# Kernel tuning notes

Hardware: AMD Instinct MI355X
Metric: run time of the kernel (lower is better)

## Reference

```python
import jax, jax.numpy as jnp
import numpy as np

B, T, C, H = 4, 2048, 1024, 1024

def setup_inputs() -> dict:
    key = jax.random.key(0)
    ks = jax.random.split(key, 7)
    s = 0.02
    return {
        "x": jax.random.normal(ks[0], (B, T, C), dtype=jnp.float32),
        "k": jax.random.normal(ks[1], (B, T, C), dtype=jnp.float32),
        "q": jax.random.normal(ks[2], (B, T, C), dtype=jnp.float32),
        "v": jax.random.normal(ks[3], (B, T, C), dtype=jnp.float32),
        "Wk": jax.random.normal(ks[4], (C, H), dtype=jnp.float32) * s,
        "Wq": jax.random.normal(ks[5], (C, H), dtype=jnp.float32) * s,
        "Wv": jax.random.normal(ks[6], (C, H), dtype=jnp.float32) * s,
    }

def reference(x, k, q, v, Wk, Wq, Wv):
    Tcur = x.shape[1]
    kp = jnp.einsum('btc,ch->bth', k, Wk)
    qp = jnp.einsum('btc,ch->bth', q, Wq)
    # NOTE: original torch code (faithfully) projects v with the QUERY weights
    vp = jnp.einsum('btc,ch->bth', v, Wq)
    scale = jnp.asarray(H, jnp.float32) ** -0.5
    weights = jnp.einsum('bth,bsh->bts', qp, kp) * scale  # [B,T,T]
    causal = jnp.tril(jnp.ones((Tcur, Tcur), dtype=bool))
    weights = jnp.where(causal, weights, -jnp.inf)
    weights = jax.nn.softmax(weights, axis=-1)
    # dropout p=0.0 -> identity
    out = jnp.einsum('bts,bsh->bth', weights, vp)
    return out
```

## Files before the change

### kernel.cpp

```cpp
#include <hip/hip_runtime.h>
#include <stdint.h>
#include <math.h>

typedef unsigned short u16;
typedef __attribute__((ext_vector_type(8))) short short8;
typedef __attribute__((ext_vector_type(8))) u16 ushort8;
typedef __attribute__((ext_vector_type(4))) u16 u16x4;
typedef __attribute__((ext_vector_type(4))) float floatx4;

__device__ __forceinline__ u16 f2bf(float f) {
  union { float f; unsigned u; } c; c.f = f;
  unsigned u = c.u;
  return (u16)((u + 0x7fffu + ((u >> 16) & 1u)) >> 16);
}
__device__ __forceinline__ float bf2f(u16 h) {
  union { unsigned u; float f; } c; c.u = (unsigned)h << 16;
  return c.f;
}

__device__ __forceinline__ void async16(const u16* g, u16* l) {
  auto* gp = reinterpret_cast<const __attribute__((address_space(1))) uint32_t*>(
      reinterpret_cast<uintptr_t>(g));
  auto* lp = reinterpret_cast<__attribute__((address_space(3))) uint32_t*>(
      reinterpret_cast<uintptr_t>(l));
  __builtin_amdgcn_global_load_lds(gp, lp, 16, 0, 0);
}

#define WAIT_VM4 0xF74
#define WAIT_VM0 0xF70

template <int OUT_BF16>
__global__ __launch_bounds__(256) void gemm_bt(
    const u16* __restrict__ A, const u16* __restrict__ B, void* __restrict__ Cv,
    int K, int lda, int ldb, int ldc,
    long long sA, long long sB, long long sC,
    float scale, int tri_grid, int causal_klimit, int rev_m,
    int vpt, u16* __restrict__ vpC) {
  int bm, bn;
  if (tri_grid) {
    const int bx = blockIdx.x;
    int i = (int)((sqrtf(8.f * bx + 1.f) - 1.f) * 0.5f);
    while ((i + 1) * (i + 2) / 2 <= bx) ++i;
    while (i * (i + 1) / 2 > bx) --i;
    bm = i;
    bn = bx - i * (i + 1) / 2;
  } else {
    bm = rev_m ? ((int)gridDim.x - 1 - (int)blockIdx.x) : (int)blockIdx.x;
    bn = blockIdx.y;
  }
  const int m0 = bm * 128;
  const int n0 = bn * 128;
  A += (size_t)blockIdx.z * sA;
  B += (size_t)blockIdx.z * sB;

  __shared__ u16 As[2][4096];
  __shared__ u16 Bs[2][4096];

  const int tid = threadIdx.x;
  const int lane = tid & 63;
  const int wid = tid >> 6;
  const int wm = (wid & 1) * 64;
  const int wn = (wid >> 1) * 64;
  const int fr = lane & 15;
  const int fq = lane >> 4;

  floatx4 acc[4][4] = {};

  int kt_end = K >> 5;
  if (causal_klimit) {
    int lim = (m0 >> 5) + 4;
    if (lim < kt_end) kt_end = lim;
  }

  const int rowi = tid >> 2;
  const int segi = tid & 3;
  const int sgz = segi ^ ((rowi >> 1) & 3);
  const u16* gA = A + (size_t)(m0 + rowi) * lda + sgz * 8;
  const u16* gB = B + (size_t)(n0 + rowi) * ldb + sgz * 8;

  int offA[4], offB[4];
#pragma unroll
  for (int i = 0; i < 4; ++i) {
    int ra = wm + i * 16 + fr;
    offA[i] = ra * 32 + (fq ^ ((ra >> 1) & 3)) * 8;
    int rb = wn + i * 16 + fr;
    offB[i] = rb * 32 + (fq ^ ((rb >> 1) & 3)) * 8;
  }

  auto issue = [&](int kt) {
    const int k0 = kt << 5;
    const int odd = kt & 1;
    async16(gA + k0, &As[odd][tid * 8]);
    async16(gA + k0 + (size_t)64 * lda, &As[odd][tid * 8 + 2048]);
    async16(gB + k0, &Bs[odd][tid * 8]);
    async16(gB + k0 + (size_t)64 * ldb, &Bs[odd][tid * 8 + 2048]);
  };

  issue(0);
  for (int kt = 0; kt < kt_end; ++kt) {
    if (kt + 1 < kt_end) {
      issue(kt + 1);
      __builtin_amdgcn_s_waitcnt(WAIT_VM4);
    } else {
      __builtin_amdgcn_s_waitcnt(WAIT_VM0);
    }
    asm volatile("s_barrier" ::: "memory");

    const u16* ab = As[kt & 1];
    const u16* bb = Bs[kt & 1];
    short8 av[4], bv[4];
#pragma unroll
    for (int i = 0; i < 4; ++i) av[i] = *(const short8*)(ab + offA[i]);
#pragma unroll
    for (int j = 0; j < 4; ++j) bv[j] = *(const short8*)(bb + offB[j]);

#pragma unroll
    for (int i = 0; i < 4; ++i)
#pragma unroll
      for (int j = 0; j < 4; ++j)
        acc[i][j] = __builtin_amdgcn_mfma_f32_16x16x32_bf16(av[i], bv[j],
                                                            acc[i][j], 0, 0, 0);
    asm volatile("s_barrier" ::: "memory");
  }

  if (vpt && blockIdx.z == 2) {
#pragma unroll
    for (int i = 0; i < 4; ++i) {
      const int m = m0 + wm + i * 16 + fq * 4;
      const int b = m >> 11, t = m & 2047;
#pragma unroll
      for (int j = 0; j < 4; ++j) {
        const int n = n0 + wn + j * 16 + fr;
        u16x4 o;
#pragma unroll
        for (int r = 0; r < 4; ++r) o[r] = f2bf(acc[i][j][r]);
        *(u16x4*)&vpC[(size_t)b * 2097152 + (size_t)n * 2048 + t] = o;
      }
    }
    return;
  }
  if (OUT_BF16) {
    u16* C = (u16*)Cv + (size_t)blockIdx.z * sC;
#pragma unroll
    for (int i = 0; i < 4; ++i) {
      const int m = m0 + wm + i * 16 + fq * 4;
#pragma unroll
      for (int j = 0; j < 4; ++j) {
        const int n = n0 + wn + j * 16 + fr;
#pragma unroll
        for (int r = 0; r < 4; ++r)
          C[(size_t)(m + r) * ldc + n] = f2bf(acc[i][j][r] * scale);
      }
    }
  } else {
    float* C = (float*)Cv + (size_t)blockIdx.z * sC;
#pragma unroll
    for (int i = 0; i < 4; ++i) {
      const int m = m0 + wm + i * 16 + fq * 4;
#pragma unroll
      for (int j = 0; j < 4; ++j) {
        const int n = n0 + wn + j * 16 + fr;
#pragma unroll
        for (int r = 0; r < 4; ++r)
          C[(size_t)(m + r) * ldc + n] = acc[i][j][r] * scale;
      }
    }
  }
}

__global__ __launch_bounds__(512, 2) void gemm_bt_256(
    const u16* __restrict__ A, const u16* __restrict__ B,
    u16* __restrict__ Cb, int K, int lda, int ldb, int ldc,
    long long sA, long long sB, long long sC, u16* __restrict__ vpC) {
  const int m0 = blockIdx.x * 256;
  const int n0 = blockIdx.y * 256;
  A += (size_t)blockIdx.z * sA;
  B += (size_t)blockIdx.z * sB;

  __shared__ u16 lds[2][32768];

  const int tid = threadIdx.x;
  const int lane = tid & 63;
  const int wid = tid >> 6;
  const int wr = wid & 1;
  const int wc = wid >> 1;
  const int fr = lane & 15;
  const int fq = lane >> 4;

  floatx4 acc[8][4] = {};
  const int NT = K >> 6;

  const int srow = tid >> 3;
  const int sseg = (tid & 7) ^ (srow & 7);
  const u16* gA = A + (size_t)(m0 + srow) * lda + sseg * 8;
  const u16* gB = B + (size_t)(n0 + srow) * ldb + sseg * 8;
  const int ldst = tid * 8;

  auto stageA = [&](int h, int t) {
    u16* d = &lds[t & 1][h * 8192 + ldst];
    const u16* s = gA + (size_t)(h * 128) * lda + t * 64;
    async16(s, d);
    async16(s + (size_t)64 * lda, d + 4096);
  };
  auto stageB = [&](int h, int t) {
    u16* d = &lds[t & 1][16384 + h * 8192 + ldst];
    const u16* s = gB + (size_t)(h * 128) * ldb + t * 64;
    async16(s, d);
    async16(s + (size_t)64 * ldb, d + 4096);
  };

  int aoff[2], boff[2];
#pragma unroll
  for (int s = 0; s < 2; ++s) {
    const int seg = ((((s << 2) + fq) ^ (fr & 7))) * 8;
    aoff[s] = wr * 8192 + fr * 64 + seg;
    boff[s] = 16384 + (wc >> 1) * 8192 + (wc & 1) * 4096 + fr * 64 + seg;
  }

  stageA(0, 0); stageA(1, 0); stageB(0, 0); stageB(1, 0);
  stageB(0, 1); stageB(1, 1);
  __builtin_amdgcn_s_waitcnt(WAIT_VM4);
  asm volatile("s_barrier" ::: "memory");

  short8 a[4][2], b0[2][2], b1[2][2];
  for (int t = 0; t < NT; ++t) {
    const u16* L = lds[t & 1];

#pragma unroll
    for (int i = 0; i < 4; ++i)
#pragma unroll
      for (int s = 0; s < 2; ++s)
        a[i][s] = *(const short8*)(L + aoff[s] + i * 1024);
#pragma unroll
    for (int j = 0; j < 2; ++j)
#pragma unroll
      for (int s = 0; s < 2; ++s)
        b0[j][s] = *(const short8*)(L + boff[s] + j * 1024);
    if (t + 1 < NT) stageA(0, t + 1);
    asm volatile("s_barrier" ::: "memory");
    __builtin_amdgcn_s_setprio(1);
#pragma unroll
    for (int i = 0; i < 4; ++i)
#pragma unroll
      for (int j = 0; j < 2; ++j) {
        acc[i][j] = __builtin_amdgcn_mfma_f32_16x16x32_bf16(
            a[i][0], b0[j][0], acc[i][j], 0, 0, 0);
        acc[i][j] = __builtin_amdgcn_mfma_f32_16x16x32_bf16(
            a[i][1], b0[j][1], acc[i][j], 0, 0, 0);
      }
    __builtin_amdgcn_s_setprio(0);
    asm volatile("s_barrier" ::: "memory");

#pragma unroll
    for (int j = 0; j < 2; ++j)
#pragma unroll
      for (int s = 0; s < 2; ++s)
        b1[j][s] = *(const short8*)(L + boff[s] + (2 + j) * 1024);
    if (t + 1 < NT) stageA(1, t + 1);
    asm volatile("s_barrier" ::: "memory");
    __builtin_amdgcn_s_setprio(1);
#pragma unroll
    for (int i = 0; i < 4; ++i)
#pragma unroll
      for (int j = 0; j < 2; ++j) {
        acc[i][2 + j] = __builtin_amdgcn_mfma_f32_16x16x32_bf16(
            a[i][0], b1[j][0], acc[i][2 + j], 0, 0, 0);
        acc[i][2 + j] = __builtin_amdgcn_mfma_f32_16x16x32_bf16(
            a[i][1], b1[j][1], acc[i][2 + j], 0, 0, 0);
      }
    __builtin_amdgcn_s_setprio(0);
    asm volatile("s_barrier" ::: "memory");

#pragma unroll
    for (int i = 0; i < 4; ++i)
#pragma unroll
      for (int s = 0; s < 2; ++s)
        a[i][s] = *(const short8*)(L + aoff[s] + (4 + i) * 1024);
    if (t + 2 < NT) stageB(0, t + 2);
    asm volatile("s_barrier" ::: "memory");
    __builtin_amdgcn_s_setprio(1);
#pragma unroll
    for (int i = 0; i < 4; ++i)
#pragma unroll
      for (int j = 0; j < 2; ++j) {
        acc[4 + i][j] = __builtin_amdgcn_mfma_f32_16x16x32_bf16(
            a[i][0], b0[j][0], acc[4 + i][j], 0, 0, 0);
        acc[4 + i][j] = __builtin_amdgcn_mfma_f32_16x16x32_bf16(
            a[i][1], b0[j][1], acc[4 + i][j], 0, 0, 0);
      }
    __builtin_amdgcn_s_setprio(0);
    asm volatile("s_barrier" ::: "memory");

    if (t + 2 < NT) {
      stageB(1, t + 2);
      __builtin_amdgcn_s_waitcnt(WAIT_VM4);
    } else {
      __builtin_amdgcn_s_waitcnt(WAIT_VM0);
    }
    asm volatile("s_barrier" ::: "memory");
    __builtin_amdgcn_s_setprio(1);
#pragma unroll
    for (int i = 0; i < 4; ++i)
#pragma unroll
      for (int j = 0; j < 2; ++j) {
        acc[4 + i][2 + j] = __builtin_amdgcn_mfma_f32_16x16x32_bf16(
            a[i][0], b1[j][0], acc[4 + i][2 + j], 0, 0, 0);
        acc[4 + i][2 + j] = __builtin_amdgcn_mfma_f32_16x16x32_bf16(
            a[i][1], b1[j][1], acc[4 + i][2 + j], 0, 0, 0);
      }
    __builtin_amdgcn_s_setprio(0);
    asm volatile("s_barrier" ::: "memory");
  }

  const int mBase = m0 + wr * 128;
  const int nBase = n0 + wc * 64;
  if (blockIdx.z == 2) {
#pragma unroll
    for (int i = 0; i < 8; ++i) {
      const int m = mBase + i * 16 + fq * 4;
      const int b = m >> 11, tt = m & 2047;
#pragma unroll
      for (int j = 0; j < 4; ++j) {
        const int n = nBase + j * 16 + fr;
        u16x4 o;
#pragma unroll
        for (int r = 0; r < 4; ++r) o[r] = f2bf(acc[i][j][r]);
        *(u16x4*)&vpC[(size_t)b * 2097152 + (size_t)n * 2048 + tt] = o;
      }
    }
  } else {
    u16* Co = Cb + (size_t)blockIdx.z * sC;
#pragma unroll
    for (int i = 0; i < 8; ++i) {
      const int m = mBase + i * 16 + fq * 4;
#pragma unroll
      for (int j = 0; j < 4; ++j) {
        const int n = nBase + j * 16 + fr;
#pragma unroll
        for (int r = 0; r < 4; ++r)
          Co[(size_t)(m + r) * ldc + n] = f2bf(acc[i][j][r]);
      }
    }
  }
}

__global__ __launch_bounds__(256) void cast3(
    const float* __restrict__ q, const float* __restrict__ k,
    const float* __restrict__ v, u16* __restrict__ out, int n8) {
  int i = blockIdx.x * 256 + threadIdx.x;
  if (i >= n8) return;
  const float* src = blockIdx.y == 0 ? q : (blockIdx.y == 1 ? k : v);
  u16* dst = out + (size_t)blockIdx.y * n8 * 8;
  floatx4 a = ((const floatx4*)src)[i * 2];
  floatx4 b = ((const floatx4*)src)[i * 2 + 1];
  ushort8 o;
#pragma unroll
  for (int j = 0; j < 4; ++j) { o[j] = f2bf(a[j]); o[4 + j] = f2bf(b[j]); }
  ((ushort8*)dst)[i] = o;
}

__global__ __launch_bounds__(256) void transpose_castW(
    const float* __restrict__ Wq, const float* __restrict__ Wk,
    u16* __restrict__ out, int R, int C) {
  __shared__ u16 tile[64][72];
  const float* in = (blockIdx.z == 1) ? Wk : Wq;
  u16* dst = out + (size_t)blockIdx.z * R * C;
  const int r0 = blockIdx.x * 64;
  const int c0 = blockIdx.y * 64;
  const int tid = threadIdx.x;
#pragma unroll
  for (int rnd = 0; rnd < 2; ++rnd) {
    int e = rnd * 256 + tid;
    int rr = e >> 3, seg = e & 7;
    const float* p = &in[(size_t)(r0 + rr) * C + c0 + seg * 8];
    floatx4 a = *(const floatx4*)p;
    floatx4 b = *(const floatx4*)(p + 4);
    u16* tp = &tile[rr][seg * 8];
#pragma unroll
    for (int j = 0; j < 4; ++j) { tp[j] = f2bf(a[j]); tp[4 + j] = f2bf(b[j]); }
  }
  __syncthreads();
#pragma unroll
  for (int rnd = 0; rnd < 2; ++rnd) {
    int e = rnd * 256 + tid;
    int cc = e >> 3, rseg = e & 7;
    ushort8 tv;
#pragma unroll
    for (int j = 0; j < 8; ++j) tv[j] = tile[rseg * 8 + j][cc];
    *(ushort8*)&dst[(size_t)(c0 + cc) * R + r0 + rseg * 8] = tv;
  }
}

__global__ __launch_bounds__(256) void softmax_causal(u16* __restrict__ S,
                                                      int T) {
  const int row = blockIdx.x;
  const int t = row & (T - 1);
  const int len = t + 1;
  u16* srow = S + (size_t)row * T;
  const int tid = threadIdx.x;

  float vals[8];
  int cnt = 0;
  float mx = -1e30f;
  for (int i = tid; i < len; i += 256) {
    float v = bf2f(srow[i]);
    vals[cnt++] = v;
    mx = fmaxf(mx, v);
  }
  __shared__ float red[4];
#pragma unroll
  for (int o = 32; o > 0; o >>= 1) mx = fmaxf(mx, __shfl_down(mx, o, 64));
  if ((tid & 63) == 0) red[tid >> 6] = mx;
  __syncthreads();
  mx = fmaxf(fmaxf(red[0], red[1]), fmaxf(red[2], red[3]));
  __syncthreads();

  float sum = 0.f;
  for (int c = 0; c < cnt; ++c) {
    vals[c] = __expf(vals[c] - mx);
    sum += vals[c];
  }
#pragma unroll
  for (int o = 32; o > 0; o >>= 1) sum += __shfl_down(sum, o, 64);
  if ((tid & 63) == 0) red[tid >> 6] = sum;
  __syncthreads();
  sum = red[0] + red[1] + red[2] + red[3];
  const float inv = 1.f / sum;

  int c = 0;
  for (int i = tid; i < len; i += 256) srow[i] = f2bf(vals[c++] * inv);
  for (int i = tid; i < T; i += 256)
    if (i >= len) srow[i] = 0;
}

extern "C" void kernel_launch(void* const* d_in, const int* in_sizes, int n_in,
                              void* d_out, int out_size, void* d_ws,
                              size_t ws_size, hipStream_t stream) {
  (void)in_sizes; (void)n_in; (void)out_size; (void)ws_size;
  const float* k  = (const float*)d_in[1];
  const float* q  = (const float*)d_in[2];
  const float* v  = (const float*)d_in[3];
  const float* Wk = (const float*)d_in[4];
  const float* Wq = (const float*)d_in[5];
  float* out = (float*)d_out;

  const int B = 4, T = 2048, C = 1024, H = 1024;
  const int M = B * T;
  const size_t MC = (size_t)M * C, CH = (size_t)C * H, MH = (size_t)M * H;

  u16* qkv  = (u16*)d_ws;
  u16* WT   = qkv + 3 * MC;
  u16* qkvp = WT + 3 * CH;
  u16* vpT  = qkvp + 2 * MH;
  u16* Sb   = vpT + MH;

  const int n8 = (int)(MC / 8);
  cast3<<<dim3(n8 / 256, 3), 256, 0, stream>>>(q, k, v, qkv, n8);
  transpose_castW<<<dim3(C / 64, H / 64, 3), 256, 0, stream>>>(Wq, Wk, WT, C, H);

  gemm_bt_256<<<dim3(M / 256, H / 256, 3), 512, 0, stream>>>(
      qkv, WT, qkvp, C, C, C, H,
      (long long)MC, (long long)CH, (long long)MH, vpT);

  gemm_bt<1><<<dim3(136, 1, B), 256, 0, stream>>>(
      qkvp, qkvp + MH, Sb, H, H, H, T,
      (long long)T * H, (long long)T * H, (long long)T * T,
      0.03125f, 1, 0, 0, 0, nullptr);

  softmax_causal<<<dim3(B * T), 256, 0, stream>>>(Sb, T);

  gemm_bt<0><<<dim3(T / 128, H / 128, B), 256, 0, stream>>>(
      Sb, vpT, out, T, T, T, H,
      (long long)T * T, (long long)H * T, (long long)T * H,
      1.f, 0, 1, 1, 0, nullptr);
}
```

Baseline: 338.2 us.

## Use 256-tile causal GEMMs for attention and 128-tile GEMM for projections

Swaps which GEMM kernel handles each stage. The QKV projection now uses the 128x128 kernel, and both attention GEMMs use a templated 256x256 kernel. The QK^T kernel skips upper-triangle tiles, and the PV kernel limits its K loop to the causal range. Softmax only zeroes padding up to the next 256 boundary instead of the full row. The aim is more data reuse per tile in the attention matmuls. The cost is far fewer blocks in flight (144 and 128 blocks of 512 threads) and uneven per-block work, which may leave compute units idle. The projection also loses the larger-tile kernel.

```diff
diff --git a/kernel.cpp b/kernel.cpp
--- a/kernel.cpp
+++ b/kernel.cpp
@@ -34,20 +34,9 @@
     const u16* __restrict__ A, const u16* __restrict__ B, void* __restrict__ Cv,
     int K, int lda, int ldb, int ldc,
     long long sA, long long sB, long long sC,
-    float scale, int tri_grid, int causal_klimit, int rev_m,
-    int vpt, u16* __restrict__ vpC) {
-  int bm, bn;
-  if (tri_grid) {
-    const int bx = blockIdx.x;
-    int i = (int)((sqrtf(8.f * bx + 1.f) - 1.f) * 0.5f);
-    while ((i + 1) * (i + 2) / 2 <= bx) ++i;
-    while (i * (i + 1) / 2 > bx) --i;
-    bm = i;
-    bn = bx - i * (i + 1) / 2;
-  } else {
-    bm = rev_m ? ((int)gridDim.x - 1 - (int)blockIdx.x) : (int)blockIdx.x;
-    bn = blockIdx.y;
-  }
+    float scale, int vpt, u16* __restrict__ vpC) {
+  const int bm = blockIdx.x;
+  const int bn = blockIdx.y;
   const int m0 = bm * 128;
   const int n0 = bn * 128;
   A += (size_t)blockIdx.z * sA;
@@ -66,11 +55,7 @@
 
   floatx4 acc[4][4] = {};
 
-  int kt_end = K >> 5;
-  if (causal_klimit) {
-    int lim = (m0 >> 5) + 4;
-    if (lim < kt_end) kt_end = lim;
-  }
+  const int kt_end = K >> 5;
 
   const int rowi = tid >> 2;
   const int segi = tid & 3;
@@ -168,12 +153,18 @@
   }
 }
 
-__global__ __launch_bounds__(512, 2) void gemm_bt_256(
-    const u16* __restrict__ A, const u16* __restrict__ B,
-    u16* __restrict__ Cb, int K, int lda, int ldb, int ldc,
-    long long sA, long long sB, long long sC, u16* __restrict__ vpC) {
-  const int m0 = blockIdx.x * 256;
-  const int n0 = blockIdx.y * 256;
+template <int MODE>
+__global__ __launch_bounds__(512, 2) void gemm256(
+    const u16* __restrict__ A, const u16* __restrict__ B, void* __restrict__ Cv,
+    int K, int lda, int ldb, int ldc,
+    long long sA, long long sB, long long sC, float scale) {
+  const int r = blockIdx.x & 7;
+  const int s = blockIdx.x >> 3;
+  if (MODE == 0 && s > r) return;
+  const int bm = r;
+  const int bn = s;
+  const int m0 = bm * 256;
+  const int n0 = bn * 256;
   A += (size_t)blockIdx.z * sA;
   B += (size_t)blockIdx.z * sB;
 
@@ -188,7 +179,7 @@
   const int fq = lane >> 4;
 
   floatx4 acc[8][4] = {};
-  const int NT = K >> 6;
+  const int NT = (MODE == 1) ? ((m0 + 256) >> 6) : (K >> 6);
 
   const int srow = tid >> 3;
   const int sseg = (tid & 7) ^ (srow & 7);
@@ -198,23 +189,23 @@
 
   auto stageA = [&](int h, int t) {
     u16* d = &lds[t & 1][h * 8192 + ldst];
-    const u16* s = gA + (size_t)(h * 128) * lda + t * 64;
-    async16(s, d);
-    async16(s + (size_t)64 * lda, d + 4096);
+    const u16* src = gA + (size_t)(h * 128) * lda + t * 64;
+    async16(src, d);
+    async16(src + (size_t)64 * lda, d + 4096);
   };
   auto stageB = [&](int h, int t) {
     u16* d = &lds[t & 1][16384 + h * 8192 + ldst];
-    const u16* s = gB + (size_t)(h * 128) * ldb + t * 64;
-    async16(s, d);
-    async16(s + (size_t)64 * ldb, d + 4096);
+    const u16* src = gB + (size_t)(h * 128) * ldb + t * 64;
+    async16(src, d);
+    async16(src + (size_t)64 * ldb, d + 4096);
   };
 
   int aoff[2], boff[2];
 #pragma unroll
-  for (int s = 0; s < 2; ++s) {
-    const int seg = ((((s << 2) + fq) ^ (fr & 7))) * 8;
-    aoff[s] = wr * 8192 + fr * 64 + seg;
-    boff[s] = 16384 + (wc >> 1) * 8192 + (wc & 1) * 4096 + fr * 64 + seg;
+  for (int sg = 0; sg < 2; ++sg) {
+    const int seg = ((((sg << 2) + fq) ^ (fr & 7))) * 8;
+    aoff[sg] = wr * 8192 + fr * 64 + seg;
+    boff[sg] = 16384 + (wc >> 1) * 8192 + (wc & 1) * 4096 + fr * 64 + seg;
   }
 
   stageA(0, 0); stageA(1, 0); stageB(0, 0); stageB(1, 0);
@@ -229,13 +220,13 @@
 #pragma unroll
     for (int i = 0; i < 4; ++i)
 #pragma unroll
-      for (int s = 0; s < 2; ++s)
-        a[i][s] = *(const short8*)(L + aoff[s] + i * 1024);
+      for (int sg = 0; sg < 2; ++sg)
+        a[i][sg] = *(const short8*)(L + aoff[sg] + i * 1024);
 #pragma unroll
     for (int j = 0; j < 2; ++j)
 #pragma unroll
-      for (int s = 0; s < 2; ++s)
-        b0[j][s] = *(const short8*)(L + boff[s] + j * 1024);
+      for (int sg = 0; sg < 2; ++sg)
+        b0[j][sg] = *(const short8*)(L + boff[sg] + j * 1024);
     if (t + 1 < NT) stageA(0, t + 1);
     asm volatile("s_barrier" ::: "memory");
     __builtin_amdgcn_s_setprio(1);
@@ -254,8 +245,8 @@
 #pragma unroll
     for (int j = 0; j < 2; ++j)
 #pragma unroll
-      for (int s = 0; s < 2; ++s)
-        b1[j][s] = *(const short8*)(L + boff[s] + (2 + j) * 1024);
+      for (int sg = 0; sg < 2; ++sg)
+        b1[j][sg] = *(const short8*)(L + boff[sg] + (2 + j) * 1024);
     if (t + 1 < NT) stageA(1, t + 1);
     asm volatile("s_barrier" ::: "memory");
     __builtin_amdgcn_s_setprio(1);
@@ -274,8 +265,8 @@
 #pragma unroll
     for (int i = 0; i < 4; ++i)
 #pragma unroll
-      for (int s = 0; s < 2; ++s)
-        a[i][s] = *(const short8*)(L + aoff[s] + (4 + i) * 1024);
+      for (int sg = 0; sg < 2; ++sg)
+        a[i][sg] = *(const short8*)(L + aoff[sg] + (4 + i) * 1024);
     if (t + 2 < NT) stageB(0, t + 2);
     asm volatile("s_barrier" ::: "memory");
     __builtin_amdgcn_s_setprio(1);
@@ -314,22 +305,21 @@
 
   const int mBase = m0 + wr * 128;
   const int nBase = n0 + wc * 64;
-  if (blockIdx.z == 2) {
+  if (MODE == 0) {
+    u16* Co = (u16*)Cv + (size_t)blockIdx.z * sC;
 #pragma unroll
     for (int i = 0; i < 8; ++i) {
       const int m = mBase + i * 16 + fq * 4;
-      const int b = m >> 11, tt = m & 2047;
 #pragma unroll
       for (int j = 0; j < 4; ++j) {
         const int n = nBase + j * 16 + fr;
-        u16x4 o;
-#pragma unroll
-        for (int r = 0; r < 4; ++r) o[r] = f2bf(acc[i][j][r]);
-        *(u16x4*)&vpC[(size_t)b * 2097152 + (size_t)n * 2048 + tt] = o;
+#pragma unroll
+        for (int rg = 0; rg < 4; ++rg)
+          Co[(size_t)(m + rg) * ldc + n] = f2bf(acc[i][j][rg] * scale);
       }
     }
   } else {
-    u16* Co = Cb + (size_t)blockIdx.z * sC;
+    float* Co = (float*)Cv + (size_t)blockIdx.z * sC;
 #pragma unroll
     for (int i = 0; i < 8; ++i) {
       const int m = mBase + i * 16 + fq * 4;
@@ -337,8 +327,8 @@
       for (int j = 0; j < 4; ++j) {
         const int n = nBase + j * 16 + fr;
 #pragma unroll
-        for (int r = 0; r < 4; ++r)
-          Co[(size_t)(m + r) * ldc + n] = f2bf(acc[i][j][r]);
+        for (int rg = 0; rg < 4; ++rg)
+          Co[(size_t)(m + rg) * ldc + n] = acc[i][j][rg] * scale;
       }
     }
   }
@@ -429,7 +419,8 @@
 
   int c = 0;
   for (int i = tid; i < len; i += 256) srow[i] = f2bf(vals[c++] * inv);
-  for (int i = tid; i < T; i += 256)
+  const int zlim = ((t >> 8) + 1) << 8;
+  for (int i = tid; i < zlim; i += 256)
     if (i >= len) srow[i] = 0;
 }
 
@@ -458,19 +449,17 @@
   cast3<<<dim3(n8 / 256, 3), 256, 0, stream>>>(q, k, v, qkv, n8);
   transpose_castW<<<dim3(C / 64, H / 64, 3), 256, 0, stream>>>(Wq, Wk, WT, C, H);
 
-  gemm_bt_256<<<dim3(M / 256, H / 256, 3), 512, 0, stream>>>(
+  gemm_bt<1><<<dim3(M / 128, H / 128, 3), 256, 0, stream>>>(
       qkv, WT, qkvp, C, C, C, H,
-      (long long)MC, (long long)CH, (long long)MH, vpT);
-
-  gemm_bt<1><<<dim3(136, 1, B), 256, 0, stream>>>(
+      (long long)MC, (long long)CH, (long long)MH, 1.f, 1, vpT);
+
+  gemm256<0><<<dim3(64, 1, B), 512, 0, stream>>>(
       qkvp, qkvp + MH, Sb, H, H, H, T,
-      (long long)T * H, (long long)T * H, (long long)T * T,
-      0.03125f, 1, 0, 0, 0, nullptr);
+      (long long)T * H, (long long)T * H, (long long)T * T, 0.03125f);
 
   softmax_causal<<<dim3(B * T), 256, 0, stream>>>(Sb, T);
 
-  gemm_bt<0><<<dim3(T / 128, H / 128, B), 256, 0, stream>>>(
+  gemm256<1><<<dim3(32, 1, B), 512, 0, stream>>>(
       Sb, vpT, out, T, T, T, H,
-      (long long)T * T, (long long)H * T, (long long)T * H,
-      1.f, 0, 1, 1, 0, nullptr);
-}
+      (long long)T * T, (long long)H * T, (long long)T * H, 1.f);
+}
```

Measured after the change: 344.9 us. About the same (+2.0%).
